# Performance work log

Hardware: AMD Instinct MI355X
Metric: run time of the kernel (lower is better)

The kernel has to match this reference:

```python
import jax, jax.numpy as jnp
import numpy as np

ATT_DIM = 512
HEADS = 8
HEAD_DIM = ATT_DIM // HEADS
D_IN = 512
LEFT_MASK = 256
RIGHT_MASK = 0
LARGE = 1e30


def pos_encoding(S, d):
    # Transformer-XL sinusoid table over relative positions S-1 .. -(S-1), length 2S-1.
    inv_freq = (1.0 / (10000.0 ** (np.arange(0, d, 2.0) / d))).astype(np.float32)
    pos = jnp.arange(S - 1, -S, -1, dtype=jnp.float32)          # [2S-1]
    ang = pos[:, None] * jnp.asarray(inv_freq)[None, :]          # [2S-1, d/2]
    # concat([sin, cos], -1) on a trailing singleton -> interleaved sin/cos per frequency
    return jnp.stack([jnp.sin(ang), jnp.cos(ang)], axis=-1).reshape(2 * S - 1, d)


def rel_shift(x):
    # x: [B, N, S, 2S-1] -> [B, N, S, S] with out[i, j] = x[i, S-1 - i + j]
    B, N, S, L = x.shape
    x = jnp.pad(x, ((0, 0), (0, 0), (0, 0), (1, 0)))             # [B,N,S,L+1]
    x = x.reshape(B, N, L + 1, S)[:, :, 1:, :]                   # [B,N,L,S]
    x = x.reshape(B, N, S, L)
    return x[:, :, :, :S]


def setup_inputs() -> dict:
    key = jax.random.key(0)
    ks = jax.random.split(key, 9)
    B, S, D = 2, 2048, D_IN
    scale = 0.02
    return {
        "x": jax.random.normal(ks[0], (B, S, D), dtype=jnp.float32),
        "Wq": jax.random.normal(ks[1], (D, ATT_DIM), dtype=jnp.float32) * scale,
        "b_con": jax.random.normal(ks[2], (ATT_DIM,), dtype=jnp.float32) * scale,
        "b_rel": jax.random.normal(ks[3], (ATT_DIM,), dtype=jnp.float32) * scale,
        "Wk": jax.random.normal(ks[4], (D, ATT_DIM), dtype=jnp.float32) * scale,
        "Wkr": jax.random.normal(ks[5], (D_IN, ATT_DIM), dtype=jnp.float32) * scale,
        "Wv": jax.random.normal(ks[6], (D, ATT_DIM), dtype=jnp.float32) * scale,
        "bv": jax.random.normal(ks[7], (ATT_DIM,), dtype=jnp.float32) * scale,
        "x_len": jax.random.randint(ks[8], (B,), 1, S + 1).astype(jnp.int32),
    }


def reference(x, Wq, b_con, b_rel, Wk, Wkr, Wv, bv, x_len):
    B, S, D = x.shape
    N, Dh = HEADS, HEAD_DIM

    # content/relative query share the kernel (TiedDense) with separate biases
    q_lin = jnp.einsum('bsd,de->bse', x, Wq)
    q_con = (q_lin + b_con).reshape(B, S, N, Dh)
    q_rel = (q_lin + b_rel).reshape(B, S, N, Dh)
    k_con = jnp.einsum('bsd,de->bse', x, Wk).reshape(B, S, N, Dh)

    content_energy = jnp.einsum('bind,bjnd->bnij', q_con, k_con)  # [B,N,S,S]

    pos_emb = pos_encoding(S, D_IN)                               # [2S-1, D]
    k_rel = (pos_emb @ Wkr).reshape(2 * S - 1, N, Dh)
    relative_energy = jnp.einsum('bind,jnd->bnij', q_rel, k_rel)  # [B,N,S,2S-1]
    relative_energy = rel_shift(relative_energy)                  # [B,N,S,S]

    energy = (content_energy + relative_energy) / jnp.sqrt(jnp.float32(Dh))

    # sequence mask over keys (broadcast [B,1,1,S]) * banded mask (band_part)
    j = jnp.arange(S)
    seq_mask = (j[None, :] < x_len[:, None]).astype(jnp.float32)[:, None, None, :]
    i = jnp.arange(S)[:, None]
    band = ((i - j[None, :] <= LEFT_MASK) & (j[None, :] - i <= RIGHT_MASK)).astype(jnp.float32)
    mask = seq_mask * band[None, None, :, :]

    masked_energy = energy - (1.0 - mask) * LARGE
    attention = jax.nn.softmax(masked_energy, axis=-1)

    v = (jnp.einsum('bsd,de->bse', x, Wv) + bv).reshape(B, S, N, Dh)
    context = jnp.einsum('bnij,bjnd->bind', attention, v).reshape(B, S, N * Dh)
    return context
```

## Files before the change

### kernel.cpp

```cpp
#include <hip/hip_runtime.h>
#include <math.h>

#define S_ 2048
#define NH 8
#define LP 72
#define RP 328

typedef __attribute__((ext_vector_type(8))) short short8;
typedef __attribute__((ext_vector_type(4))) float f32x4;
typedef unsigned short ushort_t;

__device__ __forceinline__ short bf16r(float x) {
    union { float f; unsigned u; } v; v.f = x;
    unsigned r = v.u + 0x7fffu + ((v.u >> 16) & 1u);
    return (short)(r >> 16);
}
__device__ __forceinline__ float b2f(ushort_t h) {
    union { float f; unsigned u; } v; v.u = ((unsigned)h) << 16; return v.f;
}

__global__ __launch_bounds__(256) void prep_kernel(
    const float* __restrict__ x,
    const float* __restrict__ Wq, const float* __restrict__ Wk,
    const float* __restrict__ Wv, const float* __restrict__ Wkr,
    const int* __restrict__ xlen_p,
    ushort_t* __restrict__ WTq, ushort_t* __restrict__ WTk,
    ushort_t* __restrict__ WTv, ushort_t* __restrict__ WTkr,
    ushort_t* __restrict__ pos, ushort_t* __restrict__ xb16,
    float* __restrict__ xpart)
{
    const int widx = blockIdx.z;
    const int t = threadIdx.x;
    if (widx == 4) {
        const int base = blockIdx.y * 8 + blockIdx.x;
        const float C = -0.051905126482615036f;
        const int f = t;
#pragma unroll
        for (int rep = 0; rep < 6; ++rep) {
            const int r = base + rep * 64;
            unsigned pk = 0;
            if (r <= 256) {
                float ang = (float)r * exp2f(C * (float)f);
                unsigned s = (unsigned)(ushort_t)bf16r(sinf(ang));
                unsigned c = (unsigned)(ushort_t)bf16r(cosf(ang));
                pk = s | (c << 16);
            }
            ((unsigned*)pos)[(size_t)r * 256 + f] = pk;
        }
        return;
    }
    if (widx == 5) {
        const int sub = blockIdx.y * 8 + blockIdx.x;
        {
            const int b = sub >> 5, s0 = (sub & 31) * 64;
            if (s0 >= xlen_p[b] + 383) return;
        }
        const size_t base = (size_t)sub * 32768;
#pragma unroll
        for (int it = 0; it < 8; ++it) {
            const size_t idx = base + (size_t)it * 4096 + (size_t)t * 16;
            const float* src = &x[idx];
            ushort_t t16[16];
#pragma unroll
            for (int u = 0; u < 16; ++u) t16[u] = (ushort_t)bf16r(src[u]);
            *(short8*)&xb16[idx]     = *(short8*)&t16[0];
            *(short8*)&xb16[idx + 8] = *(short8*)&t16[8];
        }
        return;
    }
    if (widx == 6) {
        const int sub = blockIdx.y * 8 + blockIdx.x;
        const int b = sub >> 5, rb = sub & 31;
        const float* src = &x[((size_t)b * 2048 + (size_t)rb * 64) * 512];
        float s0 = 0.f, s1 = 0.f;
        for (int r = 0; r < 64; ++r) {
            s0 += src[(size_t)r * 512 + t];
            s1 += src[(size_t)r * 512 + t + 256];
        }
        xpart[(size_t)sub * 512 + t]       = s0;
        xpart[(size_t)sub * 512 + t + 256] = s1;
        return;
    }
    const float* W = (widx == 0) ? Wq : (widx == 1) ? Wk : (widx == 2) ? Wv : Wkr;
    ushort_t* WT   = (widx == 0) ? WTq : (widx == 1) ? WTk : (widx == 2) ? WTv : WTkr;
    const int k0 = blockIdx.x * 64, n0 = blockIdx.y * 64;
    __shared__ __align__(16) ushort_t T[64][72];
    const int srow = t >> 2, sc0 = (t & 3) * 16;
    const float* src = &W[(size_t)(k0 + srow) * 512 + n0 + sc0];
#pragma unroll
    for (int u = 0; u < 16; ++u) T[sc0 + u][srow] = (ushort_t)bf16r(src[u]);
    __syncthreads();
    ushort_t* dst = &WT[(size_t)(n0 + srow) * 512 + k0 + sc0];
    *(short8*)dst       = *(const short8*)&T[srow][sc0];
    *(short8*)(dst + 8) = *(const short8*)&T[srow][sc0 + 8];
}

__global__ __launch_bounds__(256) void qkv_gemm(
    const ushort_t* __restrict__ xb16,
    const ushort_t* __restrict__ WTq, const ushort_t* __restrict__ WTk,
    const ushort_t* __restrict__ WTv,
    const ushort_t* __restrict__ pos, const ushort_t* __restrict__ WTkr,
    const float* __restrict__ b_con, const float* __restrict__ b_rel,
    const float* __restrict__ bv, const int* __restrict__ xlen_p,
    const float* __restrict__ xpart,
    ushort_t* __restrict__ qcon, ushort_t* __restrict__ qrel,
    ushort_t* __restrict__ kout, ushort_t* __restrict__ vT,
    ushort_t* __restrict__ krel, float* __restrict__ vmean)
{
    const int widx = blockIdx.y >> 3;
    const int tid = threadIdx.x, lane = tid & 63, w = tid >> 6;
    const int quad = lane >> 4, l16 = lane & 15;

    __shared__ __align__(16) ushort_t A_lds[2][128][40];
    __shared__ __align__(16) ushort_t B_lds[2][64][40];

    f32x4 acc[2][4];
#pragma unroll
    for (int mt = 0; mt < 2; ++mt)
#pragma unroll
        for (int nt = 0; nt < 4; ++nt) acc[mt][nt] = (f32x4){0.f, 0.f, 0.f, 0.f};

    const int arow = tid >> 1, ak0 = (tid & 1) * 16;
    const int brow = tid >> 2, bk0 = (tid & 3) * 8;

    const ushort_t* Asrc;
    const ushort_t* Bsrc;

    if (widx < 2) {
        const int m0 = blockIdx.x * 128;
        {
            const int xl = xlen_p[m0 >> 11];
            const int s0 = m0 & 2047;
            if (widx == 0) { if (s0 >= xl + 256) return; }
            else           { if (s0 >= xl + 63)  return; }
        }
        const int n0 = (blockIdx.y & 7) * 64;
        const ushort_t* WT = (widx == 0) ? WTq : WTk;
        Asrc = &xb16[(size_t)(m0 + arow) * 512 + ak0];
        Bsrc = &WT[(size_t)(n0 + brow) * 512 + bk0];
    } else if (widx == 2) {
        const int vb = (blockIdx.y & 7) * 32 + blockIdx.x;
        const int m0d = (vb & 3) * 128;
        const int n0j = (vb >> 2) * 64;
        {
            const int xl = xlen_p[n0j >> 11];
            if ((n0j & 2047) >= xl + 63) return;
        }
        Asrc = &WTv[(size_t)(m0d + arow) * 512 + ak0];
        Bsrc = &xb16[(size_t)(n0j + brow) * 512 + bk0];
    } else {
        if (blockIdx.x >= 24) {
            float* xm = (float*)A_lds;
            for (int idx = tid; idx < 1024; idx += 256) {
                const int bb = idx >> 9, k = idx & 511;
                float s = 0.f;
                for (int p = 0; p < 32; ++p)
                    s += xpart[(size_t)(bb * 32 + p) * 512 + k];
                xm[bb * 512 + k] = s * (1.0f / 2048.0f);
            }
            __syncthreads();
            if (tid < 64) {
                const int d = (blockIdx.x - 24) * 64 + tid;
                const ushort_t* wrow = &WTv[(size_t)d * 512];
                float a0 = 0.f, a1 = 0.f;
                for (int k = 0; k < 512; k += 8) {
                    short8 wv = *(const short8*)(wrow + k);
#pragma unroll
                    for (int u = 0; u < 8; ++u) {
                        const float wf = b2f((ushort_t)wv[u]);
                        a0 += xm[k + u] * wf;
                        a1 += xm[512 + k + u] * wf;
                    }
                }
                const float bvd = bv[d];
                vmean[d]       = a0 + bvd;
                vmean[512 + d] = a1 + bvd;
            }
            return;
        }
        const int m0 = (blockIdx.x >> 3) * 128;
        const int n0 = (blockIdx.x & 7) * 64;
        Asrc = &pos[(size_t)(m0 + arow) * 512 + ak0];
        Bsrc = &WTkr[(size_t)(n0 + brow) * 512 + bk0];
    }

    {
        short8 pa0 = *(const short8*)Asrc;
        short8 pa1 = *(const short8*)(Asrc + 8);
        short8 pb  = *(const short8*)Bsrc;
        *(short8*)&A_lds[0][arow][ak0]     = pa0;
        *(short8*)&A_lds[0][arow][ak0 + 8] = pa1;
        *(short8*)&B_lds[0][brow][bk0]     = pb;
        pa0 = *(const short8*)(Asrc + 32);
        pa1 = *(const short8*)(Asrc + 40);
        pb  = *(const short8*)(Bsrc + 32);
        __syncthreads();

#pragma unroll 1
        for (int it = 0; it < 16; ++it) {
            const int cur = it & 1;
            if (it < 15) {
                *(short8*)&A_lds[cur ^ 1][arow][ak0]     = pa0;
                *(short8*)&A_lds[cur ^ 1][arow][ak0 + 8] = pa1;
                *(short8*)&B_lds[cur ^ 1][brow][bk0]     = pb;
                if (it < 14) {
                    pa0 = *(const short8*)(Asrc + it * 32 + 64);
                    pa1 = *(const short8*)(Asrc + it * 32 + 72);
                    pb  = *(const short8*)(Bsrc + it * 32 + 64);
                }
            }
            short8 a0 = *(const short8*)&A_lds[cur][w * 32 + l16][quad * 8];
            short8 a1 = *(const short8*)&A_lds[cur][w * 32 + 16 + l16][quad * 8];
#pragma unroll
            for (int nt = 0; nt < 4; ++nt) {
                short8 bb = *(const short8*)&B_lds[cur][nt * 16 + l16][quad * 8];
                acc[0][nt] = __builtin_amdgcn_mfma_f32_16x16x32_bf16(a0, bb, acc[0][nt], 0, 0, 0);
                acc[1][nt] = __builtin_amdgcn_mfma_f32_16x16x32_bf16(a1, bb, acc[1][nt], 0, 0, 0);
            }
            __syncthreads();
        }
    }

    if (widx < 2) {
        const int m0 = blockIdx.x * 128;
        const int n0 = (blockIdx.y & 7) * 64;
#pragma unroll
        for (int nt = 0; nt < 4; ++nt) {
            const int col = n0 + nt * 16 + l16;
            float bc = 0.f, br = 0.f;
            if (widx == 0) { bc = b_con[col]; br = b_rel[col]; }
#pragma unroll
            for (int mt = 0; mt < 2; ++mt) {
#pragma unroll
                for (int reg = 0; reg < 4; ++reg) {
                    const size_t m = (size_t)(m0 + w * 32 + mt * 16 + quad * 4 + reg);
                    const float val = acc[mt][nt][reg];
                    if (widx == 0) {
                        qcon[m * 512 + col] = (ushort_t)bf16r((val + bc) * 0.125f);
                        qrel[m * 512 + col] = (ushort_t)bf16r((val + br) * 0.125f);
                    } else {
                        kout[m * 512 + col] = (ushort_t)bf16r(val);
                    }
                }
            }
        }
    } else if (widx == 2) {
        const int vb = (blockIdx.y & 7) * 32 + blockIdx.x;
        const int m0d = (vb & 3) * 128;
        const int n0j = (vb >> 2) * 64;
        const int b = n0j >> 11;
#pragma unroll
        for (int mt = 0; mt < 2; ++mt) {
#pragma unroll
            for (int reg = 0; reg < 4; ++reg) {
                const int d = m0d + w * 32 + mt * 16 + quad * 4 + reg;
                const int n = d >> 6, dd = d & 63;
                const float bvv = bv[d];
#pragma unroll
                for (int nt = 0; nt < 4; ++nt) {
                    const int s = (n0j + nt * 16 + l16) & 2047;
                    vT[((size_t)((b * NH + n) * 64 + dd)) * 2048 + s] =
                        (ushort_t)bf16r(acc[mt][nt][reg] + bvv);
                }
            }
        }
    } else {
        const int m0 = (blockIdx.x >> 3) * 128;
        const int n0 = (blockIdx.x & 7) * 64;
#pragma unroll
        for (int nt = 0; nt < 4; ++nt) {
            const int col = n0 + nt * 16 + l16;
#pragma unroll
            for (int mt = 0; mt < 2; ++mt)
#pragma unroll
                for (int reg = 0; reg < 4; ++reg) {
                    const size_t m = (size_t)(m0 + w * 32 + mt * 16 + quad * 4 + reg);
                    krel[m * 512 + col] = (ushort_t)bf16r(acc[mt][nt][reg]);
                }
        }
    }
}

__global__ __launch_bounds__(256) void attn_kernel(
    const ushort_t* __restrict__ qcon, const ushort_t* __restrict__ qrel,
    const ushort_t* __restrict__ kbuf, const ushort_t* __restrict__ vT,
    const ushort_t* __restrict__ krel, const float* __restrict__ vmean,
    const int* __restrict__ xlen_p, float* __restrict__ out)
{
    const int bx = blockIdx.x;
    const int tile = ((bx & 7) << 2) | (bx >> 3);
    const int n = blockIdx.y, b = blockIdx.z;
    const int i0 = tile * 64;
    const int tid = threadIdx.x, lane = tid & 63, w = tid >> 6;
    const int quad = lane >> 4, l16 = lane & 15;
    const int xlen = xlen_p[b];

    if (i0 >= xlen + 256) {
        const int row = tid >> 2, cf = (tid & 3) * 16;
        const float* vm = &vmean[(size_t)b * 512 + n * 64 + cf];
        float* dst = &out[((size_t)b * S_ + i0 + row) * 512 + n * 64 + cf];
#pragma unroll
        for (int u = 0; u < 16; u += 4)
            *(float4*)&dst[u] = *(const float4*)&vm[u];
        return;
    }
    int nchunk = (xlen - i0 + 256 + 63) >> 6;
    if (nchunk > 5) nchunk = 5;
    const int c0 = (i0 < 256) ? ((256 - i0) >> 6) : 0;

    __shared__ __align__(16) ushort_t k_lds[64][LP];
    __shared__ __align__(16) ushort_t vT_lds[64][LP];
    __shared__ __align__(16) ushort_t R_lds[64][RP];

    const int srow = tid >> 2, sc0 = (tid & 3) * 16;
    const size_t vTbase = (size_t)((b * NH + n) * 64) * 2048;

    short8 kr[2], vr[2], kn[2], vn[2];

    auto issue = [&](int c, short8* kd, short8* vd) {
        const int jc0 = i0 - 256 + c * 64;
        const ushort_t* ks = &kbuf[((size_t)b * S_ + jc0 + srow) * 512 + n * 64 + sc0];
        kd[0] = *(const short8*)ks;
        kd[1] = *(const short8*)(ks + 8);
        const ushort_t* vs = &vT[vTbase + (size_t)srow * 2048 + jc0 + sc0];
        vd[0] = *(const short8*)vs;
        vd[1] = *(const short8*)(vs + 8);
    };

    const ushort_t* qc = &qcon[((size_t)b * S_ + i0 + w * 16 + l16) * 512 + n * 64 + quad * 8];
    const short8 aq0 = *(const short8*)qc;
    const short8 aq1 = *(const short8*)(qc + 32);
    issue(c0, kr, vr);

    {
        const ushort_t* qr = &qrel[((size_t)b * S_ + i0 + w * 16 + l16) * 512 + n * 64 + quad * 8];
        const short8 ar0 = *(const short8*)qr;
        const short8 ar1 = *(const short8*)(qr + 32);
        const int rlim = (i0 + 63 < 256) ? i0 + 63 : 256;
#pragma unroll 1
        for (int rc = 0; rc <= (rlim >> 6); ++rc) {
            const ushort_t* ks = &krel[(size_t)(rc * 64 + srow) * 512 + n * 64 + sc0];
            short8 s0v = *(const short8*)ks;
            short8 s1v = *(const short8*)(ks + 8);
            __syncthreads();
            *(short8*)&k_lds[srow][sc0]     = s0v;
            *(short8*)&k_lds[srow][sc0 + 8] = s1v;
            __syncthreads();
#pragma unroll
            for (int nt = 0; nt < 4; ++nt) {
                if (rc * 64 + nt * 16 <= rlim) {
                    short8 b0 = *(const short8*)&k_lds[nt * 16 + l16][quad * 8];
                    short8 b1 = *(const short8*)&k_lds[nt * 16 + l16][quad * 8 + 32];
                    f32x4 s = (f32x4){0.f, 0.f, 0.f, 0.f};
                    s = __builtin_amdgcn_mfma_f32_16x16x32_bf16(ar0, b0, s, 0, 0, 0);
                    s = __builtin_amdgcn_mfma_f32_16x16x32_bf16(ar1, b1, s, 0, 0, 0);
                    const int r = rc * 64 + nt * 16 + l16;
#pragma unroll
                    for (int reg = 0; reg < 4; ++reg) {
                        const int rowq = w * 16 + quad * 4 + reg;
                        if (r <= 256) R_lds[rowq][rowq + 256 - r] = (ushort_t)bf16r(s[reg]);
                    }
                }
            }
        }
    }

    f32x4 Oa[4];
#pragma unroll
    for (int nt = 0; nt < 4; ++nt) Oa[nt] = (f32x4){0.f, 0.f, 0.f, 0.f};
    float lpart[4] = {};

#pragma unroll 1
    for (int c = c0; c < nchunk; ++c) {
        const int jc0 = i0 - 256 + c * 64;
        __syncthreads();
        *(short8*)&k_lds[srow][sc0]      = kr[0];
        *(short8*)&k_lds[srow][sc0 + 8]  = kr[1];
        *(short8*)&vT_lds[srow][sc0]     = vr[0];
        *(short8*)&vT_lds[srow][sc0 + 8] = vr[1];
        if (c + 1 < nchunk) issue(c + 1, kn, vn);
        __syncthreads();

        f32x4 Sacc[4];
#pragma unroll
        for (int jt = 0; jt < 4; ++jt) {
            short8 bk0 = *(const short8*)&k_lds[jt * 16 + l16][quad * 8];
            short8 bk1 = *(const short8*)&k_lds[jt * 16 + l16][quad * 8 + 32];
            f32x4 s = (f32x4){0.f, 0.f, 0.f, 0.f};
            s = __builtin_amdgcn_mfma_f32_16x16x32_bf16(aq0, bk0, s, 0, 0, 0);
            s = __builtin_amdgcn_mfma_f32_16x16x32_bf16(aq1, bk1, s, 0, 0, 0);
            Sacc[jt] = s;
        }

#pragma unroll
        for (int jt = 0; jt < 4; ++jt) {
#pragma unroll
            for (int reg = 0; reg < 4; ++reg) {
                const int row = w * 16 + quad * 4 + reg;
                const int i = i0 + row;
                const int j = jc0 + jt * 16 + l16;
                const int r = i - j;
                const bool valid = (j < xlen) && (r >= 0) && (r <= 256);
                float rvv = b2f(R_lds[row][c * 64 + jt * 16 + l16]);
                float e = valid ? __expf(Sacc[jt][reg] + rvv) : 0.f;
                lpart[reg] += e;
                R_lds[row][c * 64 + jt * 16 + l16] = (ushort_t)bf16r(e);
            }
        }

        short8 ap0 = *(const short8*)&R_lds[w * 16 + l16][c * 64 + quad * 8];
        short8 ap1 = *(const short8*)&R_lds[w * 16 + l16][c * 64 + quad * 8 + 32];
#pragma unroll
        for (int nt = 0; nt < 4; ++nt) {
            short8 bv0 = *(const short8*)&vT_lds[nt * 16 + l16][quad * 8];
            short8 bv1 = *(const short8*)&vT_lds[nt * 16 + l16][quad * 8 + 32];
            Oa[nt] = __builtin_amdgcn_mfma_f32_16x16x32_bf16(ap0, bv0, Oa[nt], 0, 0, 0);
            Oa[nt] = __builtin_amdgcn_mfma_f32_16x16x32_bf16(ap1, bv1, Oa[nt], 0, 0, 0);
        }

        kr[0] = kn[0]; kr[1] = kn[1];
        vr[0] = vn[0]; vr[1] = vn[1];
    }

#pragma unroll
    for (int reg = 0; reg < 4; ++reg) {
#pragma unroll
        for (int off = 1; off < 16; off <<= 1)
            lpart[reg] += __shfl_xor(lpart[reg], off, 64);
    }

#pragma unroll
    for (int reg = 0; reg < 4; ++reg) {
        const int i = i0 + w * 16 + quad * 4 + reg;
        const bool dead = (i >= xlen + 256);
        const float linv = 1.0f / lpart[reg];
#pragma unroll
        for (int nt = 0; nt < 4; ++nt) {
            const int d = n * 64 + nt * 16 + l16;
            float val = dead ? vmean[(size_t)b * 512 + d] : Oa[nt][reg] * linv;
            out[((size_t)b * S_ + i) * 512 + d] = val;
        }
    }
}

extern "C" void kernel_launch(void* const* d_in, const int* in_sizes, int n_in,
                              void* d_out, int out_size, void* d_ws, size_t ws_size,
                              hipStream_t stream) {
    const float* x     = (const float*)d_in[0];
    const float* Wq    = (const float*)d_in[1];
    const float* b_con = (const float*)d_in[2];
    const float* b_rel = (const float*)d_in[3];
    const float* Wk    = (const float*)d_in[4];
    const float* Wkr   = (const float*)d_in[5];
    const float* Wv    = (const float*)d_in[6];
    const float* bv    = (const float*)d_in[7];
    const int*   xlen  = (const int*)d_in[8];
    float* out = (float*)d_out;

    float* ws = (float*)d_ws;
    float* vmean = ws;
    float* xpart = vmean + 1024;
    ushort_t* ub   = (ushort_t*)(xpart + 32768);
    ushort_t* qcon = ub;
    ushort_t* kbuf = qcon + 2097152;
    ushort_t* vT   = kbuf + 2097152;
    ushort_t* qrel = vT   + 2097152;
    ushort_t* xb16 = qrel + 2097152;
    ushort_t* krel = xb16 + 2097152;
    ushort_t* pos  = krel + 196608;
    ushort_t* WTq  = pos  + 196608;
    ushort_t* WTk  = WTq + 262144;
    ushort_t* WTv  = WTk + 262144;
    ushort_t* WTkr = WTv + 262144;

    prep_kernel<<<dim3(8, 8, 7), 256, 0, stream>>>(x, Wq, Wk, Wv, Wkr, xlen,
                                                   WTq, WTk, WTv, WTkr, pos, xb16,
                                                   xpart);
    qkv_gemm<<<dim3(32, 25), 256, 0, stream>>>(xb16, WTq, WTk, WTv, pos, WTkr,
                                               b_con, b_rel, bv, xlen, xpart,
                                               qcon, qrel, kbuf, vT, krel, vmean);
    attn_kernel<<<dim3(32, 8, 2), 256, 0, stream>>>(qcon, qrel, kbuf, vT, krel,
                                                    vmean, xlen, out);
}
```

Baseline: 121.5 us.

## Fuse x column-sum into bf16 conversion and double-buffer krel loads

```diff
diff --git a/kernel.cpp b/kernel.cpp
--- a/kernel.cpp
+++ b/kernel.cpp
@@ -23,7 +23,6 @@
     const float* __restrict__ x,
     const float* __restrict__ Wq, const float* __restrict__ Wk,
     const float* __restrict__ Wv, const float* __restrict__ Wkr,
-    const int* __restrict__ xlen_p,
     ushort_t* __restrict__ WTq, ushort_t* __restrict__ WTk,
     ushort_t* __restrict__ WTv, ushort_t* __restrict__ WTkr,
     ushort_t* __restrict__ pos, ushort_t* __restrict__ xb16,
@@ -31,6 +30,10 @@
 {
     const int widx = blockIdx.z;
     const int t = threadIdx.x;
+
+    __shared__ __align__(16) ushort_t T[64][72];
+    __shared__ __align__(16) float red[8][512];
+
     if (widx == 4) {
         const int base = blockIdx.y * 8 + blockIdx.x;
         const float C = -0.051905126482615036f;
@@ -51,40 +54,42 @@
     }
     if (widx == 5) {
         const int sub = blockIdx.y * 8 + blockIdx.x;
-        {
-            const int b = sub >> 5, s0 = (sub & 31) * 64;
-            if (s0 >= xlen_p[b] + 383) return;
-        }
         const size_t base = (size_t)sub * 32768;
+        float csum[16];
+#pragma unroll
+        for (int u = 0; u < 16; ++u) csum[u] = 0.f;
 #pragma unroll
         for (int it = 0; it < 8; ++it) {
             const size_t idx = base + (size_t)it * 4096 + (size_t)t * 16;
             const float* src = &x[idx];
             ushort_t t16[16];
 #pragma unroll
-            for (int u = 0; u < 16; ++u) t16[u] = (ushort_t)bf16r(src[u]);
+            for (int u = 0; u < 16; ++u) {
+                const float f = src[u];
+                t16[u] = (ushort_t)bf16r(f);
+                csum[u] += f;
+            }
             *(short8*)&xb16[idx]     = *(short8*)&t16[0];
             *(short8*)&xb16[idx + 8] = *(short8*)&t16[8];
         }
-        return;
-    }
-    if (widx == 6) {
-        const int sub = blockIdx.y * 8 + blockIdx.x;
-        const int b = sub >> 5, rb = sub & 31;
-        const float* src = &x[((size_t)b * 2048 + (size_t)rb * 64) * 512];
-        float s0 = 0.f, s1 = 0.f;
-        for (int r = 0; r < 64; ++r) {
-            s0 += src[(size_t)r * 512 + t];
-            s1 += src[(size_t)r * 512 + t + 256];
-        }
-        xpart[(size_t)sub * 512 + t]       = s0;
-        xpart[(size_t)sub * 512 + t + 256] = s1;
+        {
+            const int g = t >> 5, c0 = (t & 31) * 16;
+#pragma unroll
+            for (int u = 0; u < 16; ++u) red[g][c0 + u] = csum[u];
+        }
+        __syncthreads();
+#pragma unroll
+        for (int c = t; c < 512; c += 256) {
+            float s = 0.f;
+#pragma unroll
+            for (int g = 0; g < 8; ++g) s += red[g][c];
+            xpart[(size_t)sub * 512 + c] = s;
+        }
         return;
     }
     const float* W = (widx == 0) ? Wq : (widx == 1) ? Wk : (widx == 2) ? Wv : Wkr;
     ushort_t* WT   = (widx == 0) ? WTq : (widx == 1) ? WTk : (widx == 2) ? WTv : WTkr;
     const int k0 = blockIdx.x * 64, n0 = blockIdx.y * 64;
-    __shared__ __align__(16) ushort_t T[64][72];
     const int srow = t >> 2, sc0 = (t & 3) * 16;
     const float* src = &W[(size_t)(k0 + srow) * 512 + n0 + sc0];
 #pragma unroll
@@ -308,9 +313,11 @@
     if (nchunk > 5) nchunk = 5;
     const int c0 = (i0 < 256) ? ((256 - i0) >> 6) : 0;
 
-    __shared__ __align__(16) ushort_t k_lds[64][LP];
-    __shared__ __align__(16) ushort_t vT_lds[64][LP];
+    __shared__ __align__(16) ushort_t kv_lds[2][64][LP];
     __shared__ __align__(16) ushort_t R_lds[64][RP];
+
+    ushort_t (*k_lds)[LP]  = kv_lds[0];
+    ushort_t (*vT_lds)[LP] = kv_lds[1];
 
     const int srow = tid >> 2, sc0 = (tid & 3) * 16;
     const size_t vTbase = (size_t)((b * NH + n) * 64) * 2048;
@@ -337,20 +344,26 @@
         const short8 ar0 = *(const short8*)qr;
         const short8 ar1 = *(const short8*)(qr + 32);
         const int rlim = (i0 + 63 < 256) ? i0 + 63 : 256;
+        const int rcmax = rlim >> 6;
+        auto kload = [&](int rc, short8& a, short8& c) {
+            const ushort_t* ks = &krel[(size_t)(rc * 64 + srow) * 512 + n * 64 + sc0];
+            a = *(const short8*)ks;
+            c = *(const short8*)(ks + 8);
+        };
+        short8 cv0, cv1, nv0, nv1;
+        kload(0, cv0, cv1);
 #pragma unroll 1
-        for (int rc = 0; rc <= (rlim >> 6); ++rc) {
-            const ushort_t* ks = &krel[(size_t)(rc * 64 + srow) * 512 + n * 64 + sc0];
-            short8 s0v = *(const short8*)ks;
-            short8 s1v = *(const short8*)(ks + 8);
-            __syncthreads();
-            *(short8*)&k_lds[srow][sc0]     = s0v;
-            *(short8*)&k_lds[srow][sc0 + 8] = s1v;
+        for (int rc = 0; rc <= rcmax; ++rc) {
+            ushort_t (*buf)[LP] = kv_lds[rc & 1];
+            *(short8*)&buf[srow][sc0]     = cv0;
+            *(short8*)&buf[srow][sc0 + 8] = cv1;
+            if (rc < rcmax) kload(rc + 1, nv0, nv1);
             __syncthreads();
 #pragma unroll
             for (int nt = 0; nt < 4; ++nt) {
                 if (rc * 64 + nt * 16 <= rlim) {
-                    short8 b0 = *(const short8*)&k_lds[nt * 16 + l16][quad * 8];
-                    short8 b1 = *(const short8*)&k_lds[nt * 16 + l16][quad * 8 + 32];
+                    short8 b0 = *(const short8*)&buf[nt * 16 + l16][quad * 8];
+                    short8 b1 = *(const short8*)&buf[nt * 16 + l16][quad * 8 + 32];
                     f32x4 s = (f32x4){0.f, 0.f, 0.f, 0.f};
                     s = __builtin_amdgcn_mfma_f32_16x16x32_bf16(ar0, b0, s, 0, 0, 0);
                     s = __builtin_amdgcn_mfma_f32_16x16x32_bf16(ar1, b1, s, 0, 0, 0);
@@ -362,6 +375,7 @@
                     }
                 }
             }
+            cv0 = nv0; cv1 = nv1;
         }
     }
 
@@ -473,7 +487,7 @@
     ushort_t* WTv  = WTk + 262144;
     ushort_t* WTkr = WTv + 262144;
 
-    prep_kernel<<<dim3(8, 8, 7), 256, 0, stream>>>(x, Wq, Wk, Wv, Wkr, xlen,
+    prep_kernel<<<dim3(8, 8, 6), 256, 0, stream>>>(x, Wq, Wk, Wv, Wkr,
                                                    WTq, WTk, WTv, WTkr, pos, xb16,
                                                    xpart);
     qkv_gemm<<<dim3(32, 25), 256, 0, stream>>>(xb16, WTq, WTk, WTv, pos, WTkr,
```

Result: no change. 123.8 us (+2.0%).
